# Kernel optimization log

Hardware: AMD Instinct MI355X
Metric: run time of the kernel (lower is better)

Reference implementation:

```python
import jax, jax.numpy as jnp
import numpy as np

NUM_ITEMS = 50000
EMB = 16
SLATE = 10
HID = 512
LAT = 64
RESP = 1024
BATCH = 256


def _linear_params(k, out_dim, in_dim):
    kw, kb = jax.random.split(k)
    s = 1.0 / np.sqrt(in_dim)
    W = jax.random.uniform(kw, (out_dim, in_dim), jnp.float32, -s, s)
    b = jax.random.uniform(kb, (out_dim,), jnp.float32, -s, s)
    return W, b


def setup_inputs() -> dict:
    key = jax.random.key(0)
    ks = jax.random.split(key, 10)
    user_repr = jax.random.randint(ks[0], (BATCH, NUM_ITEMS), 0, 2, dtype=jnp.int32)
    slate = jax.random.randint(ks[1], (BATCH, SLATE), 0, NUM_ITEMS, dtype=jnp.int32)
    response_encoded = jax.random.uniform(ks[2], (BATCH, RESP), jnp.float32)
    eps = jax.random.normal(ks[3], (BATCH, LAT), jnp.float32)
    emb = jax.random.normal(ks[4], (NUM_ITEMS, EMB), jnp.float32)
    in_enc = SLATE * EMB + EMB + RESP
    W_enc, b_enc = _linear_params(ks[5], HID, in_enc)
    W_mu, b_mu = _linear_params(ks[6], LAT, HID)
    W_lv, b_lv = _linear_params(ks[7], LAT, HID)
    in_dec = LAT + EMB + RESP
    W_d1, b_d1 = _linear_params(ks[8], HID, in_dec)
    W_d2, b_d2 = _linear_params(ks[9], SLATE * EMB, HID)
    return {"user_repr": user_repr, "slate": slate, "response_encoded": response_encoded,
            "eps": eps, "emb": emb, "W_enc": W_enc, "b_enc": b_enc,
            "W_mu": W_mu, "b_mu": b_mu, "W_lv": W_lv, "b_lv": b_lv,
            "W_d1": W_d1, "b_d1": b_d1, "W_d2": W_d2, "b_d2": b_d2}


def reference(user_repr, slate, response_encoded, eps, emb,
              W_enc, b_enc, W_mu, b_mu, W_lv, b_lv, W_d1, b_d1, W_d2, b_d2):
    # Ragged embedding-mean pooling over interacted items (vectorized segment mean):
    # mean of emb rows where user_repr==1  ==  (indicator @ emb) / count
    uf = user_repr.astype(jnp.float32)                       # [B, N]
    counts = jnp.sum(uf, axis=1, keepdims=True)              # [B, 1]
    user = (uf @ emb) / counts                               # [B, E]

    cond = jnp.concatenate([user, response_encoded], axis=1)  # [B, E+R]
    slate_emb = emb[slate]                                    # [B, K, E]
    slate_vec = slate_emb.reshape(-1, SLATE * EMB)            # [B, K*E]
    x = jnp.concatenate([slate_vec, cond], axis=1)

    # encoder
    h = jax.nn.relu(x @ W_enc.T + b_enc)
    z_mean = h @ W_mu.T + b_mu
    z_log_var = h @ W_lv.T + b_lv

    # reparameterized sample
    z = z_mean + eps * jnp.exp(0.5 * z_log_var)

    # decoder
    dz = jnp.concatenate([z, cond], axis=1)
    dh = jax.nn.relu(dz @ W_d1.T + b_d1)
    rx = jax.nn.relu(dh @ W_d2.T + b_d2)                      # [B, K*E]
    rx = rx.reshape(-1, SLATE, EMB)                           # [B, K, E]

    # scores vs all items, softmax over items
    logits = jnp.einsum('bkh,nh->bkn', rx, emb)               # [B, K, N]
    probs = jax.nn.softmax(logits, axis=2)
    recon_slate = jnp.argmax(probs, axis=2)                   # [B, K]
    recon_resp = jnp.take_along_axis(probs, slate[:, :, None], axis=2)[..., 0]  # [B, K]
    return z_mean, z_log_var, recon_slate, recon_resp
```

## Files before the change

kernel.cpp:

```cpp
#include <hip/hip_runtime.h>

#define NITEMS 50000
#define EMBD   16
#define NSLATE 10
#define HIDD   512
#define LATD   64
#define RESPD  1024
#define BATCH  256
#define PCHUNK 3125
#define LOG2E  1.44269504088896340736f
#define SHIFT  64.0f

#define NCOL   2560
#define NT     1563
#define IC     128
#define TPC    13

#define OUT_ZM 0
#define OUT_ZLV 16384
#define OUT_RS 32768
#define OUT_RR 35328

#define WS_X    0
#define WS_DZ   307200
#define WS_P2   0
#define WS_PS   0
#define WS_PM   327680
#define WS_PA   655360
#define WS_PP   589824
#define WS_PART 589824
#define WS_RX   1114112
#define WS_RXS0 1155072
#define WS_RXS1 1175552
#define WS_RXS2 1196032

typedef __attribute__((ext_vector_type(8))) short bfrag;
typedef __attribute__((ext_vector_type(16))) float f32x16;

__device__ __forceinline__ float bfround(float v) {
  unsigned u = __float_as_uint(v);
  unsigned r = (u + 0x7FFFu + ((u >> 16) & 1u)) & 0xFFFF0000u;
  return __uint_as_float(r);
}

__global__ __launch_bounds__(256) void pool_part(const int* __restrict__ u,
    const float* __restrict__ emb, float* __restrict__ pp) {
  int b = blockIdx.x, c = blockIdx.y, t = threadIdx.x;
  float acc[16];
  #pragma unroll
  for (int i = 0; i < 16; ++i) acc[i] = 0.0f;
  float cnt = 0.0f;
  const int* ub = u + (size_t)b * NITEMS;
  int n1 = c * PCHUNK + PCHUNK;
  for (int n = c * PCHUNK + t; n < n1; n += 256) {
    if (ub[n]) {
      const float4* e4 = (const float4*)(emb + (size_t)n * 16);
      float4 a = e4[0], bb = e4[1], cc = e4[2], dd = e4[3];
      acc[0] += a.x;  acc[1] += a.y;  acc[2] += a.z;  acc[3] += a.w;
      acc[4] += bb.x; acc[5] += bb.y; acc[6] += bb.z; acc[7] += bb.w;
      acc[8] += cc.x; acc[9] += cc.y; acc[10] += cc.z; acc[11] += cc.w;
      acc[12] += dd.x; acc[13] += dd.y; acc[14] += dd.z; acc[15] += dd.w;
      cnt += 1.0f;
    }
  }
  #pragma unroll
  for (int off = 32; off > 0; off >>= 1) {
    #pragma unroll
    for (int i = 0; i < 16; ++i) acc[i] += __shfl_down(acc[i], off);
    cnt += __shfl_down(cnt, off);
  }
  int lane = t & 63, wv = t >> 6;
  if (lane == 0) {
    float* dst = pp + ((size_t)(b * 16 + c) * 4 + wv) * 17;
    #pragma unroll
    for (int i = 0; i < 16; ++i) dst[i] = acc[i];
    dst[16] = cnt;
  }
}

__global__ __launch_bounds__(256) void build_x(const float* __restrict__ pp,
    const int* __restrict__ slate, const float* __restrict__ resp,
    const float* __restrict__ emb, float* __restrict__ x, float* __restrict__ dz) {
  __shared__ float fin[17];
  int b = blockIdx.x, t = threadIdx.x;
  if (t < 17) {
    float a = 0.f;
    const float* p = pp + (size_t)b * 64 * 17 + t;
    #pragma unroll
    for (int w = 0; w < 64; ++w) a += p[w * 17];
    fin[t] = a;
  }
  __syncthreads();
  float inv = 1.0f / fin[16];
  if (t < 16) {
    float uv = fin[t] * inv;
    x[b * 1200 + 160 + t] = uv;
    dz[b * 1104 + 64 + t] = uv;
  }
  if (t >= 32 && t < 192) {
    int i = t - 32;
    int k = i >> 4, e = i & 15;
    int it = slate[b * 10 + k];
    x[b * 1200 + i] = emb[(size_t)it * 16 + e];
  }
  for (int i = t; i < 1024; i += 256) {
    float r = resp[b * 1024 + i];
    x[b * 1200 + 176 + i] = r;
    dz[b * 1104 + 80 + i] = r;
  }
}

__global__ __launch_bounds__(256) void gemm64(const float* __restrict__ A,
    const float* __restrict__ B, float* __restrict__ P, int M, int N, int K, int kChunk) {
  __shared__ float As[16][68];
  __shared__ float Bs[16][68];
  int tid = threadIdx.x;
  int m0 = blockIdx.y * 64, n0 = blockIdx.x * 64;
  int ks = blockIdx.z * kChunk;
  int ke = ks + kChunk; if (ke > K) ke = K;
  int sr = tid >> 2;
  int sc = (tid & 3) * 4;
  int tx = tid & 15, ty = tid >> 4;
  float acc[4][4];
  #pragma unroll
  for (int i = 0; i < 4; ++i)
    #pragma unroll
    for (int j = 0; j < 4; ++j) acc[i][j] = 0.f;
  for (int k0 = ks; k0 < ke; k0 += 16) {
    float4 av = make_float4(0.f, 0.f, 0.f, 0.f);
    float4 bv = make_float4(0.f, 0.f, 0.f, 0.f);
    if (k0 + sc < ke)
      av = *(const float4*)(A + (size_t)(m0 + sr) * K + k0 + sc);
    if (k0 + sc < ke && n0 + sr < N)
      bv = *(const float4*)(B + (size_t)(n0 + sr) * K + k0 + sc);
    __syncthreads();
    As[sc][sr] = av.x; As[sc + 1][sr] = av.y; As[sc + 2][sr] = av.z; As[sc + 3][sr] = av.w;
    Bs[sc][sr] = bv.x; Bs[sc + 1][sr] = bv.y; Bs[sc + 2][sr] = bv.z; Bs[sc + 3][sr] = bv.w;
    __syncthreads();
    #pragma unroll
    for (int kk = 0; kk < 16; ++kk) {
      float4 a4 = *(const float4*)&As[kk][4 * ty];
      float4 b4 = *(const float4*)&Bs[kk][4 * tx];
      float a[4] = {a4.x, a4.y, a4.z, a4.w};
      float b[4] = {b4.x, b4.y, b4.z, b4.w};
      #pragma unroll
      for (int i = 0; i < 4; ++i)
        #pragma unroll
        for (int j = 0; j < 4; ++j) acc[i][j] = fmaf(a[i], b[j], acc[i][j]);
    }
  }
  float* Pz = P + (size_t)blockIdx.z * M * N;
  #pragma unroll
  for (int i = 0; i < 4; ++i) {
    int m = m0 + 4 * ty + i, n = n0 + 4 * tx;
    if (n < N)
      *(float4*)(Pz + (size_t)m * N + n) = make_float4(acc[i][0], acc[i][1], acc[i][2], acc[i][3]);
  }
}

__global__ __launch_bounds__(128) void mulv_z_kernel(const float* __restrict__ part,
    const float* __restrict__ benc,
    const float* __restrict__ Wmu, const float* __restrict__ bmu,
    const float* __restrict__ Wlv, const float* __restrict__ blv,
    const float* __restrict__ eps, float* __restrict__ out, float* __restrict__ dz) {
  __shared__ __align__(16) float hs[512];
  __shared__ float zms[64], zlvs[64];
  int b = blockIdx.x, t = threadIdx.x;
  for (int i = t; i < 512; i += 128) {
    float a = benc[i];
    #pragma unroll
    for (int s = 0; s < 4; ++s) a += part[(size_t)s * 131072 + b * 512 + i];
    hs[i] = fmaxf(a, 0.f);
  }
  __syncthreads();
  const float* Wr = (t < 64) ? (Wmu + (size_t)t * 512) : (Wlv + (size_t)(t - 64) * 512);
  float bias = (t < 64) ? bmu[t] : blv[t - 64];
  const float4* w4 = (const float4*)Wr;
  const float4* h4 = (const float4*)hs;
  float a0 = 0.f, a1 = 0.f, a2 = 0.f, a3 = 0.f;
  #pragma unroll 4
  for (int i = 0; i < 128; ++i) {
    float4 w = w4[i], hv = h4[i];
    a0 = fmaf(w.x, hv.x, a0); a1 = fmaf(w.y, hv.y, a1);
    a2 = fmaf(w.z, hv.z, a2); a3 = fmaf(w.w, hv.w, a3);
  }
  float acc = (a0 + a1) + (a2 + a3) + bias;
  if (t < 64) { out[OUT_ZM + b * 64 + t] = acc; zms[t] = acc; }
  else        { out[OUT_ZLV + b * 64 + (t - 64)] = acc; zlvs[t - 64] = acc; }
  __syncthreads();
  if (t < 64) {
    float zv = fmaf(eps[b * 64 + t], __builtin_amdgcn_exp2f(0.7213475204444817f * zlvs[t]), zms[t]);
    dz[b * 1104 + t] = zv;
  }
}

__global__ __launch_bounds__(256) void gemm_d2(const float* __restrict__ part,
    const float* __restrict__ bd1, const float* __restrict__ W, float* __restrict__ p2) {
  __shared__ float As[16][68];
  __shared__ float Bs[16][68];
  const int N = 160;
  int tid = threadIdx.x;
  int m0 = blockIdx.y * 64, n0 = blockIdx.x * 64;
  int ks = blockIdx.z * 64, ke = ks + 64;
  int sr = tid >> 2, sc = (tid & 3) * 4;
  int tx = tid & 15, ty = tid >> 4;
  float acc[4][4];
  #pragma unroll
  for (int i = 0; i < 4; ++i)
    #pragma unroll
    for (int j = 0; j < 4; ++j) acc[i][j] = 0.f;
  for (int k0 = ks; k0 < ke; k0 += 16) {
    int col = k0 + sc;
    const float* p = part + (size_t)(m0 + sr) * 512 + col;
    float4 a0 = *(const float4*)(p);
    float4 a1 = *(const float4*)(p + 131072);
    float4 a2 = *(const float4*)(p + 262144);
    float4 a3 = *(const float4*)(p + 393216);
    float4 bb = *(const float4*)(bd1 + col);
    float4 av;
    av.x = fmaxf(a0.x + a1.x + a2.x + a3.x + bb.x, 0.f);
    av.y = fmaxf(a0.y + a1.y + a2.y + a3.y + bb.y, 0.f);
    av.z = fmaxf(a0.z + a1.z + a2.z + a3.z + bb.z, 0.f);
    av.w = fmaxf(a0.w + a1.w + a2.w + a3.w + bb.w, 0.f);
    float4 bv = make_float4(0.f, 0.f, 0.f, 0.f);
    if (n0 + sr < N)
      bv = *(const float4*)(W + (size_t)(n0 + sr) * 512 + col);
    __syncthreads();
    As[sc][sr] = av.x; As[sc + 1][sr] = av.y; As[sc + 2][sr] = av.z; As[sc + 3][sr] = av.w;
    Bs[sc][sr] = bv.x; Bs[sc + 1][sr] = bv.y; Bs[sc + 2][sr] = bv.z; Bs[sc + 3][sr] = bv.w;
    __syncthreads();
    #pragma unroll
    for (int kk = 0; kk < 16; ++kk) {
      float4 a4 = *(const float4*)&As[kk][4 * ty];
      float4 b4 = *(const float4*)&Bs[kk][4 * tx];
      float a[4] = {a4.x, a4.y, a4.z, a4.w};
      float b[4] = {b4.x, b4.y, b4.z, b4.w};
      #pragma unroll
      for (int i = 0; i < 4; ++i)
        #pragma unroll
        for (int j = 0; j < 4; ++j) acc[i][j] = fmaf(a[i], b[j], acc[i][j]);
    }
  }
  float* Pz = p2 + (size_t)blockIdx.z * 40960;
  #pragma unroll
  for (int i = 0; i < 4; ++i) {
    int m = m0 + 4 * ty + i, n = n0 + 4 * tx;
    if (n < N)
      *(float4*)(Pz + (size_t)m * 160 + n) = make_float4(acc[i][0], acc[i][1], acc[i][2], acc[i][3]);
  }
}

__global__ __launch_bounds__(256) void rx_prep(const float* __restrict__ p2,
    const float* __restrict__ bd2, float* __restrict__ rx,
    unsigned short* __restrict__ rx0, unsigned short* __restrict__ rx1,
    unsigned short* __restrict__ rx2) {
  int b = blockIdx.x, t = threadIdx.x;
  if (t >= 160) return;
  float a = bd2[t];
  #pragma unroll
  for (int z = 0; z < 8; ++z) a += p2[(size_t)z * 40960 + b * 160 + t];
  float v = fmaxf(a, 0.f) * LOG2E;
  rx[b * 160 + t] = v;
  int col = b * 10 + (t >> 4), e = t & 15;
  float f0 = bfround(v);
  float d1 = v - f0;
  float f1 = bfround(d1);
  float d2 = d1 - f1;
  float f2 = bfround(d2);
  rx0[col * 16 + e] = (unsigned short)(__float_as_uint(f0) >> 16);
  rx1[col * 16 + e] = (unsigned short)(__float_as_uint(f1) >> 16);
  rx2[col * 16 + e] = (unsigned short)(__float_as_uint(f2) >> 16);
}

__global__ __launch_bounds__(256) void score_mfma(const float* __restrict__ emb,
    const unsigned short* __restrict__ rx0, const unsigned short* __restrict__ rx1,
    const unsigned short* __restrict__ rx2,
    float* __restrict__ ps, float* __restrict__ pm, int* __restrict__ pa) {
  int t = threadIdx.x;
  int w = t >> 6, l = t & 63;
  int ln = l & 31, hf = l >> 5;
  int pair = blockIdx.x * 4 + w;
  int ic = blockIdx.y;
  int colA = pair * 64 + ln;
  int colB = colA + 32;
  size_t offA = (size_t)colA * 16 + hf * 8;
  size_t offB = (size_t)colB * 16 + hf * 8;
  bfrag bA0 = *(const bfrag*)(rx0 + offA);
  bfrag bA1 = *(const bfrag*)(rx1 + offA);
  bfrag bA2 = *(const bfrag*)(rx2 + offA);
  bfrag bB0 = *(const bfrag*)(rx0 + offB);
  bfrag bB1 = *(const bfrag*)(rx1 + offB);
  bfrag bB2 = *(const bfrag*)(rx2 + offB);
  float sA = 0.f, sB = 0.f;
  float mA = -3.402823466e38f, mB = -3.402823466e38f;
  int aA = 0x7FFFFFFF, aB = 0x7FFFFFFF;
  int ts = ic * TPC, te = ts + TPC;
  if (te > NT) te = NT;
  #pragma unroll 1
  for (int tile = ts; tile < te; ++tile) {
    int r = tile * 32 + ln;
    float4 e0, e1;
    if (r < NITEMS) {
      const float4* p = (const float4*)(emb + (size_t)r * 16 + hf * 8);
      e0 = p[0]; e1 = p[1];
    } else {
      e0 = make_float4(-128.f, -128.f, -128.f, -128.f);
      e1 = e0;
    }
    float ev[8] = {e0.x, e0.y, e0.z, e0.w, e1.x, e1.y, e1.z, e1.w};
    union { bfrag f; unsigned u[4]; } A0, A1, A2;
    #pragma unroll
    for (int j = 0; j < 4; ++j) {
      float v0 = ev[2 * j], v1 = ev[2 * j + 1];
      unsigned u0 = __float_as_uint(v0), u1 = __float_as_uint(v1);
      A0.u[j] = (u0 >> 16) | (u1 & 0xFFFF0000u);
      float r0 = v0 - __uint_as_float(u0 & 0xFFFF0000u);
      float r1 = v1 - __uint_as_float(u1 & 0xFFFF0000u);
      unsigned w0 = __float_as_uint(r0), w1 = __float_as_uint(r1);
      A1.u[j] = (w0 >> 16) | (w1 & 0xFFFF0000u);
      float q0 = r0 - __uint_as_float(w0 & 0xFFFF0000u);
      float q1 = r1 - __uint_as_float(w1 & 0xFFFF0000u);
      A2.u[j] = (__float_as_uint(q0) >> 16) | (__float_as_uint(q1) & 0xFFFF0000u);
    }
    f32x16 accA, accB;
    #pragma unroll
    for (int i = 0; i < 16; ++i) { accA[i] = -SHIFT; accB[i] = -SHIFT; }
    accA = __builtin_amdgcn_mfma_f32_32x32x16_bf16(A1.f, bA1, accA, 0, 0, 0);
    accB = __builtin_amdgcn_mfma_f32_32x32x16_bf16(A1.f, bB1, accB, 0, 0, 0);
    accA = __builtin_amdgcn_mfma_f32_32x32x16_bf16(A2.f, bA0, accA, 0, 0, 0);
    accB = __builtin_amdgcn_mfma_f32_32x32x16_bf16(A2.f, bB0, accB, 0, 0, 0);
    accA = __builtin_amdgcn_mfma_f32_32x32x16_bf16(A0.f, bA2, accA, 0, 0, 0);
    accB = __builtin_amdgcn_mfma_f32_32x32x16_bf16(A0.f, bB2, accB, 0, 0, 0);
    accA = __builtin_amdgcn_mfma_f32_32x32x16_bf16(A1.f, bA0, accA, 0, 0, 0);
    accB = __builtin_amdgcn_mfma_f32_32x32x16_bf16(A1.f, bB0, accB, 0, 0, 0);
    accA = __builtin_amdgcn_mfma_f32_32x32x16_bf16(A0.f, bA1, accA, 0, 0, 0);
    accB = __builtin_amdgcn_mfma_f32_32x32x16_bf16(A0.f, bB1, accB, 0, 0, 0);
    accA = __builtin_amdgcn_mfma_f32_32x32x16_bf16(A0.f, bA0, accA, 0, 0, 0);
    accB = __builtin_amdgcn_mfma_f32_32x32x16_bf16(A0.f, bB0, accB, 0, 0, 0);
    int base = tile * 32 + 4 * hf;
    #pragma unroll
    for (int g = 0; g < 4; ++g) {
      #pragma unroll
      for (int q = 0; q < 4; ++q) {
        int idx = base + 8 * g + q;
        float xa = accA[g * 4 + q];
        sA += __builtin_amdgcn_exp2f(xa);
        if (xa > mA) { mA = xa; aA = idx; }
        float xb = accB[g * 4 + q];
        sB += __builtin_amdgcn_exp2f(xb);
        if (xb > mB) { mB = xb; aB = idx; }
      }
    }
  }
  sA += __shfl_xor(sA, 32);
  sB += __shfl_xor(sB, 32);
  float omA = __shfl_xor(mA, 32); int oaA = __shfl_xor(aA, 32);
  if (omA > mA || (omA == mA && oaA < aA)) { mA = omA; aA = oaA; }
  float omB = __shfl_xor(mB, 32); int oaB = __shfl_xor(aB, 32);
  if (omB > mB || (omB == mB && oaB < aB)) { mB = omB; aB = oaB; }
  if (hf == 0) {
    int idxA = ic * NCOL + colA;
    int idxB = ic * NCOL + colB;
    ps[idxA] = sA; pm[idxA] = mA; pa[idxA] = aA;
    ps[idxB] = sB; pm[idxB] = mB; pa[idxB] = aB;
  }
}

__global__ __launch_bounds__(256) void score_final(const float* __restrict__ psg,
    const float* __restrict__ pmg, const int* __restrict__ pag,
    const float* __restrict__ rx, const float* __restrict__ emb,
    const int* __restrict__ slate, float* __restrict__ out) {
  int tid = blockIdx.x * 256 + threadIdx.x;
  if (tid >= BATCH * 10) return;
  int b = tid / 10, k = tid % 10;
  float S = 0.f, M = -3.402823466e38f;
  int AM = 2147483647;
  for (int c = 0; c < IC; ++c) {
    int idx = c * NCOL + tid;
    S += psg[idx];
    float m2 = pmg[idx];
    int oa = pag[idx];
    bool take = (m2 > M) || (m2 == M && oa < AM);
    AM = take ? oa : AM;
    M = fmaxf(M, m2);
  }
  int it = slate[b * 10 + k];
  const float* er = emb + (size_t)it * 16;
  const float* rr = rx + b * 160 + k * 16;
  float xs = -SHIFT;
  #pragma unroll
  for (int e = 0; e < 16; ++e) xs = fmaf(rr[e], er[e], xs);
  out[OUT_RS + b * 10 + k] = (float)AM;
  out[OUT_RR + b * 10 + k] = __builtin_amdgcn_exp2f(xs) / S;
}

extern "C" void kernel_launch(void* const* d_in, const int* in_sizes, int n_in,
                              void* d_out, int out_size, void* d_ws, size_t ws_size,
                              hipStream_t stream) {
  const int* user_repr = (const int*)d_in[0];
  const int* slate = (const int*)d_in[1];
  const float* resp = (const float*)d_in[2];
  const float* eps = (const float*)d_in[3];
  const float* emb = (const float*)d_in[4];
  const float* W_enc = (const float*)d_in[5];
  const float* b_enc = (const float*)d_in[6];
  const float* W_mu = (const float*)d_in[7];
  const float* b_mu = (const float*)d_in[8];
  const float* W_lv = (const float*)d_in[9];
  const float* b_lv = (const float*)d_in[10];
  const float* W_d1 = (const float*)d_in[11];
  const float* b_d1 = (const float*)d_in[12];
  const float* W_d2 = (const float*)d_in[13];
  const float* b_d2 = (const float*)d_in[14];
  float* out = (float*)d_out;
  float* ws = (float*)d_ws;

  float* x    = ws + WS_X;
  float* dz   = ws + WS_DZ;
  float* p2   = ws + WS_P2;
  float* pp   = ws + WS_PP;
  float* part = ws + WS_PART;
  float* ps   = ws + WS_PS;
  float* pmb  = ws + WS_PM;
  int*   pab  = (int*)(ws + WS_PA);
  float* rx   = ws + WS_RX;
  unsigned short* rx0 = (unsigned short*)(ws + WS_RXS0);
  unsigned short* rx1 = (unsigned short*)(ws + WS_RXS1);
  unsigned short* rx2 = (unsigned short*)(ws + WS_RXS2);

  pool_part<<<dim3(256, 16), 256, 0, stream>>>(user_repr, emb, pp);
  build_x<<<256, 256, 0, stream>>>(pp, slate, resp, emb, x, dz);
  gemm64<<<dim3(8, 4, 4), 256, 0, stream>>>(x, W_enc, part, 256, 512, 1200, 300);
  mulv_z_kernel<<<256, 128, 0, stream>>>(part, b_enc, W_mu, b_mu, W_lv, b_lv, eps, out, dz);
  gemm64<<<dim3(8, 4, 4), 256, 0, stream>>>(dz, W_d1, part, 256, 512, 1104, 276);
  gemm_d2<<<dim3(3, 4, 8), 256, 0, stream>>>(part, b_d1, W_d2, p2);
  rx_prep<<<256, 256, 0, stream>>>(p2, b_d2, rx, rx0, rx1, rx2);
  score_mfma<<<dim3(10, IC), 256, 0, stream>>>(emb, rx0, rx1, rx2, ps, pmb, pab);
  score_final<<<10, 256, 0, stream>>>(ps, pmb, pab, rx, emb, slate, out);
}
```

Before: 281.5 us.

## Restructure pooling kernel to share embedding loads across four batch rows

The indicator-weighted pooling kernel now handles four batch rows per block and reads user_repr as int4 vectors. Each embedding row it loads is applied to all four rows with branch-free FMAs instead of a per-item conditional load. This cuts repeated embedding traffic and removes divergence. In exchange each thread holds 68 accumulator registers plus a larger shuffle reduction, and the grid drops to 640 blocks.

```diff
diff --git a/kernel.cpp b/kernel.cpp
--- a/kernel.cpp
+++ b/kernel.cpp
@@ -7,7 +7,9 @@
 #define LATD   64
 #define RESPD  1024
 #define BATCH  256
-#define PCHUNK 3125
+#define NPCH   10
+#define PI4    1250
+#define BG     4
 #define LOG2E  1.44269504088896340736f
 #define SHIFT  64.0f
 
@@ -45,36 +47,64 @@
 
 __global__ __launch_bounds__(256) void pool_part(const int* __restrict__ u,
     const float* __restrict__ emb, float* __restrict__ pp) {
-  int b = blockIdx.x, c = blockIdx.y, t = threadIdx.x;
-  float acc[16];
-  #pragma unroll
-  for (int i = 0; i < 16; ++i) acc[i] = 0.0f;
-  float cnt = 0.0f;
-  const int* ub = u + (size_t)b * NITEMS;
-  int n1 = c * PCHUNK + PCHUNK;
-  for (int n = c * PCHUNK + t; n < n1; n += 256) {
-    if (ub[n]) {
-      const float4* e4 = (const float4*)(emb + (size_t)n * 16);
-      float4 a = e4[0], bb = e4[1], cc = e4[2], dd = e4[3];
-      acc[0] += a.x;  acc[1] += a.y;  acc[2] += a.z;  acc[3] += a.w;
-      acc[4] += bb.x; acc[5] += bb.y; acc[6] += bb.z; acc[7] += bb.w;
-      acc[8] += cc.x; acc[9] += cc.y; acc[10] += cc.z; acc[11] += cc.w;
-      acc[12] += dd.x; acc[13] += dd.y; acc[14] += dd.z; acc[15] += dd.w;
-      cnt += 1.0f;
+  int bg = blockIdx.x, c = blockIdx.y, t = threadIdx.x;
+  float acc[BG][17];
+  #pragma unroll
+  for (int j = 0; j < BG; ++j)
+    #pragma unroll
+    for (int i = 0; i < 17; ++i) acc[j][i] = 0.0f;
+  const int4* ub = (const int4*)u;
+  size_t base = (size_t)(bg * BG) * 12500 + (size_t)c * PI4;
+  int nBase = c * 5000;
+  for (int i4 = t; i4 < PI4; i4 += 256) {
+    int4 u0 = ub[base + i4];
+    int4 u1 = ub[base + 12500 + i4];
+    int4 u2 = ub[base + 25000 + i4];
+    int4 u3 = ub[base + 37500 + i4];
+    int w[BG][4] = {{u0.x, u0.y, u0.z, u0.w}, {u1.x, u1.y, u1.z, u1.w},
+                    {u2.x, u2.y, u2.z, u2.w}, {u3.x, u3.y, u3.z, u3.w}};
+    const float4* e4 = (const float4*)(emb + (size_t)(nBase + i4 * 4) * 16);
+    #pragma unroll
+    for (int it = 0; it < 4; ++it) {
+      float4 ea = e4[it * 4 + 0], eb = e4[it * 4 + 1];
+      float4 ec = e4[it * 4 + 2], ed = e4[it * 4 + 3];
+      #pragma unroll
+      for (int j = 0; j < BG; ++j) {
+        float wf = (float)w[j][it];
+        acc[j][0]  = fmaf(wf, ea.x, acc[j][0]);
+        acc[j][1]  = fmaf(wf, ea.y, acc[j][1]);
+        acc[j][2]  = fmaf(wf, ea.z, acc[j][2]);
+        acc[j][3]  = fmaf(wf, ea.w, acc[j][3]);
+        acc[j][4]  = fmaf(wf, eb.x, acc[j][4]);
+        acc[j][5]  = fmaf(wf, eb.y, acc[j][5]);
+        acc[j][6]  = fmaf(wf, eb.z, acc[j][6]);
+        acc[j][7]  = fmaf(wf, eb.w, acc[j][7]);
+        acc[j][8]  = fmaf(wf, ec.x, acc[j][8]);
+        acc[j][9]  = fmaf(wf, ec.y, acc[j][9]);
+        acc[j][10] = fmaf(wf, ec.z, acc[j][10]);
+        acc[j][11] = fmaf(wf, ec.w, acc[j][11]);
+        acc[j][12] = fmaf(wf, ed.x, acc[j][12]);
+        acc[j][13] = fmaf(wf, ed.y, acc[j][13]);
+        acc[j][14] = fmaf(wf, ed.z, acc[j][14]);
+        acc[j][15] = fmaf(wf, ed.w, acc[j][15]);
+        acc[j][16] += wf;
+      }
     }
   }
   #pragma unroll
   for (int off = 32; off > 0; off >>= 1) {
     #pragma unroll
-    for (int i = 0; i < 16; ++i) acc[i] += __shfl_down(acc[i], off);
-    cnt += __shfl_down(cnt, off);
+    for (int j = 0; j < BG; ++j)
+      #pragma unroll
+      for (int i = 0; i < 17; ++i) acc[j][i] += __shfl_down(acc[j][i], off);
   }
   int lane = t & 63, wv = t >> 6;
   if (lane == 0) {
-    float* dst = pp + ((size_t)(b * 16 + c) * 4 + wv) * 17;
-    #pragma unroll
-    for (int i = 0; i < 16; ++i) dst[i] = acc[i];
-    dst[16] = cnt;
+    float* dst = pp + (size_t)((bg * NPCH + c) * 4 + wv) * (BG * 17);
+    #pragma unroll
+    for (int j = 0; j < BG; ++j)
+      #pragma unroll
+      for (int i = 0; i < 17; ++i) dst[j * 17 + i] = acc[j][i];
   }
 }
 
@@ -84,10 +114,11 @@
   __shared__ float fin[17];
   int b = blockIdx.x, t = threadIdx.x;
   if (t < 17) {
+    int bg = b >> 2, j = b & 3;
     float a = 0.f;
-    const float* p = pp + (size_t)b * 64 * 17 + t;
-    #pragma unroll
-    for (int w = 0; w < 64; ++w) a += p[w * 17];
+    const float* p = pp + (size_t)(bg * NPCH * 4) * (BG * 17) + j * 17 + t;
+    #pragma unroll
+    for (int w = 0; w < NPCH * 4; ++w) a += p[(size_t)w * (BG * 17)];
     fin[t] = a;
   }
   __syncthreads();
@@ -428,7 +459,7 @@
   unsigned short* rx1 = (unsigned short*)(ws + WS_RXS1);
   unsigned short* rx2 = (unsigned short*)(ws + WS_RXS2);
 
-  pool_part<<<dim3(256, 16), 256, 0, stream>>>(user_repr, emb, pp);
+  pool_part<<<dim3(64, NPCH), 256, 0, stream>>>(user_repr, emb, pp);
   build_x<<<256, 256, 0, stream>>>(pp, slate, resp, emb, x, dz);
   gemm64<<<dim3(8, 4, 4), 256, 0, stream>>>(x, W_enc, part, 256, 512, 1200, 300);
   mulv_z_kernel<<<256, 128, 0, stream>>>(part, b_enc, W_mu, b_mu, W_lv, b_lv, eps, out, dz);
```

Measured after the change: 276.1 us. About the same (-1.9%).
